# Optimization experiments

Measured on AMD Instinct MI355X. Metric: run time of the kernel, lower is better.

Reference implementation:

```python
import jax, jax.numpy as jnp
import numpy as np

N, D, BINS = 32768, 32, 16
SPLIT = D // 2                      # pyro spline_coupling default split
D2 = D - SPLIT
HID = 10 * D                        # pyro DenseNN default hidden dims
POUT = D2 * (3 * BINS + BINS - 1)   # widths, heights, derivatives, lambdas
BOUND = 3.0
MBW = 1e-3; MBH = 1e-3; MD = 1e-3; ML = 0.025
LOG2PI = float(np.log(2.0 * np.pi))


def _knots(lengths, lo, hi):
    # lengths [..., B] (positive, sums to 1) -> bin lengths and knot positions in [lo, hi]
    k = jnp.cumsum(lengths, axis=-1)
    k = jnp.concatenate([jnp.zeros_like(k[..., :1]), k], axis=-1)
    k = (hi - lo) * k + lo
    k = k.at[..., 0].set(lo)
    k = k.at[..., -1].set(hi)
    return k[..., 1:] - k[..., :-1], k


def rls_inverse(y, w_raw, h_raw, d_raw, l_raw):
    """Inverse monotonic rational-LINEAR spline (pyro order='linear').
    y: [N, Dp]; raw params broadcastable to [N, Dp, BINS] ([..., BINS-1] for d_raw).
    Returns x = spline^{-1}(y) and elementwise log|dx/dy|."""
    B = w_raw.shape[-1]
    w = MBW + (1.0 - MBW * B) * jax.nn.softmax(w_raw, axis=-1)
    h = MBH + (1.0 - MBH * B) * jax.nn.softmax(h_raw, axis=-1)
    d = MD + jax.nn.softplus(d_raw)
    lam = ML + (1.0 - 2.0 * ML) * jax.nn.sigmoid(l_raw)
    widths, cumw = _knots(w, -BOUND, BOUND)
    heights, cumh = _knots(h, -BOUND, BOUND)
    pad = jnp.full(d.shape[:-1] + (1,), 1.0 - MD, d.dtype)   # boundary derivatives
    d = jnp.concatenate([pad, d, pad], axis=-1)              # [..., B+1]

    bc = lambda t: jnp.broadcast_to(t, y.shape + (t.shape[-1],))
    widths, cumw, heights, cumh, d, lam = (bc(t) for t in (widths, cumw, heights, cumh, d, lam))

    inside = (y >= -BOUND) & (y <= BOUND)
    yc = jnp.clip(y, -BOUND, BOUND)
    # bin search on the y-knots (inverse pass)
    idx = jnp.clip(jnp.sum(yc[..., None] >= cumh, axis=-1) - 1, 0, B - 1)[..., None]
    take = lambda t: jnp.take_along_axis(t, idx, axis=-1)[..., 0]
    iw, icw, ih, ich = take(widths), take(cumw), take(heights), take(cumh)
    idel = ih / iw
    il = take(lam)
    idv, idvp1 = take(d[..., :-1]), take(d[..., 1:])

    wb = jnp.sqrt(idv / idvp1)                               # wa == 1
    wc = (il * idv + (1.0 - il) * wb * idvp1) / idel
    ya = ich
    yb = ih + ich
    ym = ((1.0 - il) * ya + il * wb * yb) / ((1.0 - il) + il * wb)

    left = yc <= ym
    num = jnp.where(left, il * (ya - yc),
                    (wc - il * wb) * yc + il * wb * yb - wc * ym)
    den = jnp.where(left, (wc - 1.0) * yc + ya - wc * ym,
                    (wc - wb) * yc + wb * yb - wc * ym)
    x = (num / den) * iw + icw
    dnum = jnp.where(left, wc * il * (ym - ya), wb * wc * (1.0 - il) * (yb - ym)) * iw
    ladj = jnp.log(dnum) - 2.0 * jnp.log(jnp.abs(den))
    return jnp.where(inside, x, y), jnp.where(inside, ladj, 0.0)


def coupling_inverse(y, lw, lh, ld, ll, W1, b1, W2, b2, W3, b3):
    y1, y2 = y[:, :SPLIT], y[:, SPLIT:]
    x1, l1 = rls_inverse(y1, lw, lh, ld, ll)                 # unconditional lower spline
    hdn = jax.nn.relu(x1 @ W1 + b1)
    hdn = jax.nn.relu(hdn @ W2 + b2)
    p = hdn @ W3 + b3                                        # hypernet -> upper spline params
    s0 = D2 * BINS; s1 = 2 * D2 * BINS; s2 = s1 + D2 * (BINS - 1)
    wr = p[:, :s0].reshape(-1, D2, BINS)
    hr = p[:, s0:s1].reshape(-1, D2, BINS)
    dr = p[:, s1:s2].reshape(-1, D2, BINS - 1)
    lr = p[:, s2:].reshape(-1, D2, BINS)
    x2, l2 = rls_inverse(y2, wr, hr, dr, lr)
    return jnp.concatenate([x1, x2], axis=-1), l1.sum(-1) + l2.sum(-1)


def _log_prob(data_samples, ds_means, ds_stds,
              t1_w, t1_h, t1_d, t1_l, t1_W1, t1_b1, t1_W2, t1_b2, t1_W3, t1_b3,
              t2_w, t2_h, t2_d, t2_l, t2_W1, t2_b1, t2_W2, t2_b2, t2_W3, t2_b3):
    scale = 10.0 * ds_stds
    z2 = (data_samples - ds_means) / scale                   # invert AffineTransform
    lp_aff = -jnp.sum(jnp.log(scale))                        # log|dz2/dy|
    z1, a2 = coupling_inverse(z2, t2_w, t2_h, t2_d, t2_l, t2_W1, t2_b1, t2_W2, t2_b2, t2_W3, t2_b3)
    z0, a1 = coupling_inverse(z1, t1_w, t1_h, t1_d, t1_l, t1_W1, t1_b1, t1_W2, t1_b2, t1_W3, t1_b3)
    base = -0.5 * jnp.sum(z0 * z0, axis=-1) - 0.5 * D * LOG2PI
    return base + a1 + a2 + lp_aff


def setup_inputs() -> dict:
    key = jax.random.key(0)
    ks = jax.random.split(key, 8)
    inp = {}
    inp["data_samples"] = jax.random.normal(ks[0], (N, D), jnp.float32)
    inp["ds_means"] = jax.random.normal(ks[1], (D,), jnp.float32)
    inp["ds_stds"] = jax.random.uniform(ks[2], (D,), jnp.float32, 0.5, 1.5)

    def spline_params(k):
        k1, k2, k3, k4 = jax.random.split(k, 4)
        return (0.5 * jax.random.normal(k1, (SPLIT, BINS), jnp.float32),
                0.5 * jax.random.normal(k2, (SPLIT, BINS), jnp.float32),
                0.5 * jax.random.normal(k3, (SPLIT, BINS - 1), jnp.float32),
                0.5 * jax.random.normal(k4, (SPLIT, BINS), jnp.float32))

    def nn_params(k):
        k1, k2, k3 = jax.random.split(k, 3)
        return (jax.random.normal(k1, (SPLIT, HID), jnp.float32) / np.sqrt(SPLIT),
                jnp.zeros((HID,), jnp.float32),
                jax.random.normal(k2, (HID, HID), jnp.float32) / np.sqrt(HID),
                jnp.zeros((HID,), jnp.float32),
                0.1 * jax.random.normal(k3, (HID, POUT), jnp.float32) / np.sqrt(HID),
                jnp.zeros((POUT,), jnp.float32))

    for t, ks_, kn_ in (("t1", ks[3], ks[5]), ("t2", ks[4], ks[6])):
        w, h, d, l = spline_params(ks_)
        inp[t + "_w"], inp[t + "_h"], inp[t + "_d"], inp[t + "_l"] = w, h, d, l
        W1, b1, W2, b2, W3, b3 = nn_params(kn_)
        inp[t + "_W1"], inp[t + "_b1"] = W1, b1
        inp[t + "_W2"], inp[t + "_b2"] = W2, b2
        inp[t + "_W3"], inp[t + "_b3"] = W3, b3
    return inp


def reference(data_samples, ds_means, ds_stds,
              t1_w, t1_h, t1_d, t1_l, t1_W1, t1_b1, t1_W2, t1_b2, t1_W3, t1_b3,
              t2_w, t2_h, t2_d, t2_l, t2_W1, t2_b1, t2_W2, t2_b2, t2_W3, t2_b3):
    return _log_prob(data_samples, ds_means, ds_stds,
                     t1_w, t1_h, t1_d, t1_l, t1_W1, t1_b1, t1_W2, t1_b2, t1_W3, t1_b3,
                     t2_w, t2_h, t2_d, t2_l, t2_W1, t2_b1, t2_W2, t2_b2, t2_W3, t2_b3)
```

## Files before the change

kernel.cpp:

```cpp
#include <hip/hip_runtime.h>
#include <math.h>

#define NROWS 32768
#define DD 32
#define HID 320
#define NBINS 16
#define BOUNDF 3.0f
#define MBWF 0.001f
#define MBHF 0.001f
#define MDF 0.001f
#define MLF 0.025f
#define LOG2PIF 1.8378770664093453f

#define WS_LP 0
#define WS_TBL 16
#define TBL_STRIDE 112
#define WS_B3P 4096
#define W2T_BYTE 32768
#define W3T_BYTE 442368

typedef __attribute__((ext_vector_type(8))) unsigned short ushort8_t;
typedef __attribute__((ext_vector_type(8))) __bf16 bf16x8;
typedef __attribute__((ext_vector_type(4))) float f32x4;

__device__ __forceinline__ unsigned short f2bf(float x) {
    unsigned u = __builtin_bit_cast(unsigned, x);
    return (unsigned short)((u + 0x7FFFu + ((u >> 16) & 1u)) >> 16);
}
__device__ __forceinline__ float bf2f(unsigned short s) {
    return __builtin_bit_cast(float, (unsigned)s << 16);
}
__device__ __forceinline__ f32x4 mfma_bf16(ushort8_t a, ushort8_t b, f32x4 c) {
    return __builtin_amdgcn_mfma_f32_16x16x32_bf16(
        __builtin_bit_cast(bf16x8, a), __builtin_bit_cast(bf16x8, b), c, 0, 0, 0);
}

__device__ __forceinline__ float softplus_precise(float x) {
    return (x > 0.f) ? (x + log1pf(expf(-x))) : log1pf(expf(x));
}
__device__ __forceinline__ float softplus_fast(float x) {
    return fmaxf(x, 0.f) + __logf(1.f + __expf(-fabsf(x)));
}

__device__ __forceinline__ void rls_core(float y, float iw, float icw, float ih, float ich,
                                         float il, float idv, float idvp1,
                                         float* xo, float* lo_) {
    bool inside = (y >= -BOUNDF) && (y <= BOUNDF);
    float yc = fminf(fmaxf(y, -BOUNDF), BOUNDF);
    float idel = ih / iw;
    float wb = sqrtf(idv / idvp1);
    float wc = (il * idv + (1.f - il) * wb * idvp1) / idel;
    float ya = ich;
    float yb = ih + ich;
    float ym = ((1.f - il) * ya + il * wb * yb) / ((1.f - il) + il * wb);
    bool left = (yc <= ym);
    float num = left ? (il * (ya - yc)) : ((wc - il * wb) * yc + il * wb * yb - wc * ym);
    float den = left ? ((wc - 1.f) * yc + ya - wc * ym) : ((wc - wb) * yc + wb * yb - wc * ym);
    float x = num / den * iw + icw;
    float dnum = (left ? (wc * il * (ym - ya)) : (wb * wc * (1.f - il) * (yb - ym))) * iw;
    float ladj = __logf(dnum) - 2.f * __logf(fabsf(den));
    *xo = inside ? x : y;
    *lo_ = inside ? ladj : 0.f;
}

__device__ __forceinline__ int colmap(int np) {
    int j = np >> 6, s = np & 63;
    if (s < 16) return j * 16 + s;
    if (s < 32) return 256 + j * 16 + (s - 16);
    if (s < 47) return 512 + j * 15 + (s - 32);
    if (s == 47) return -1;
    return 752 + j * 16 + (s - 48);
}

__global__ void prep_tables(const float* __restrict__ t1w, const float* __restrict__ t1h,
                            const float* __restrict__ t1d, const float* __restrict__ t1l,
                            const float* __restrict__ t2w, const float* __restrict__ t2h,
                            const float* __restrict__ t2d, const float* __restrict__ t2l,
                            const float* __restrict__ stds, float* __restrict__ ws) {
    int td = threadIdx.x;
    if (td == 32) {
        float lp = 0.f;
        for (int k = 0; k < DD; ++k) lp -= logf(10.f * stds[k]);
        ws[WS_LP] = lp;
    }
    if (td < 32) {
        int c = td >> 4, j = td & 15;
        const float* wr = (c == 0 ? t1w : t2w) + j * NBINS;
        const float* hr = (c == 0 ? t1h : t2h) + j * NBINS;
        const float* dr = (c == 0 ? t1d : t2d) + j * (NBINS - 1);
        const float* lr = (c == 0 ? t1l : t2l) + j * NBINS;
        float* tb = ws + WS_TBL + (c * 16 + j) * TBL_STRIDE;
        float mw = -1e30f, mh = -1e30f;
        for (int b = 0; b < NBINS; ++b) { mw = fmaxf(mw, wr[b]); mh = fmaxf(mh, hr[b]); }
        float sw = 0.f, sh = 0.f;
        for (int b = 0; b < NBINS; ++b) { sw += expf(wr[b] - mw); sh += expf(hr[b] - mh); }
        float fw = (1.f - NBINS * MBWF) / sw;
        float fh = (1.f - NBINS * MBHF) / sh;
        float kx[17], ky[17];
        kx[0] = -BOUNDF; ky[0] = -BOUNDF;
        float cw = 0.f, ch = 0.f;
        for (int b = 0; b < NBINS; ++b) {
            cw += MBWF + fw * expf(wr[b] - mw);
            ch += MBHF + fh * expf(hr[b] - mh);
            kx[b + 1] = 2.f * BOUNDF * cw - BOUNDF;
            ky[b + 1] = 2.f * BOUNDF * ch - BOUNDF;
        }
        kx[16] = BOUNDF; ky[16] = BOUNDF;
        for (int b = 0; b < 17; ++b) { tb[b] = ky[b]; tb[17 + b] = kx[b]; }
        tb[34] = 1.f - MDF;
        for (int b = 1; b <= 15; ++b) tb[34 + b] = MDF + softplus_precise(dr[b - 1]);
        tb[50] = 1.f - MDF;
        for (int b = 0; b < NBINS; ++b) {
            tb[51 + b] = kx[b + 1] - kx[b];
            tb[67 + b] = ky[b + 1] - ky[b];
            tb[83 + b] = MLF + (1.f - 2.f * MLF) / (1.f + expf(-lr[b]));
        }
    }
}

__global__ void prep_weights(const float* __restrict__ t2W2, const float* __restrict__ t1W2,
                             const float* __restrict__ t2W3, const float* __restrict__ t1W3,
                             const float* __restrict__ t2b3, const float* __restrict__ t1b3,
                             unsigned short* __restrict__ w2t, unsigned short* __restrict__ w3t,
                             float* __restrict__ b3p) {
    int id = blockIdx.x * 512 + threadIdx.x;
    if (id < 204800) {
        int c = id / 102400;
        int rem = id - c * 102400;
        int k = rem / 320, n = rem - k * 320;
        const float* W2 = c ? t1W2 : t2W2;
        w2t[c * 102400 + n * 320 + k] = f2bf(W2[k * 320 + n]);
    } else if (id < 860160) {
        int id2 = id - 204800;
        int c = id2 / 327680;
        int rem = id2 - c * 327680;
        int k = rem / 1024, np = rem - k * 1024;
        int col = colmap(np);
        const float* W3 = c ? t1W3 : t2W3;
        w3t[(size_t)c * 327680 + (size_t)np * 320 + k] =
            f2bf(col < 0 ? 0.f : W3[(size_t)k * 1008 + col]);
    } else if (id < 862208) {
        int idb = id - 860160;
        int c = idb / 1024, np = idb - c * 1024;
        int col = colmap(np);
        const float* b3 = c ? t1b3 : t2b3;
        b3p[c * 1024 + np] = (col < 0) ? 0.f : b3[col];
    }
}

__device__ __forceinline__ void coupling(
        int t, float (*zs)[33], float* lacc,
        unsigned short* h1b, unsigned short* h2b, unsigned short* pts,
        const float* __restrict__ tbl,
        const float* __restrict__ W1, const float* __restrict__ b1,
        const unsigned short* __restrict__ w2t, const float* __restrict__ b2,
        const unsigned short* __restrict__ w3t, const float* __restrict__ b3p) {
    const int l = t & 63, w = t >> 6;
    const int wm = w >> 2, wn = w & 3;

#pragma unroll
    for (int rep = 0; rep < 2; ++rep) {
        int row = (t >> 4) + rep * 32, jd = t & 15;
        float y1 = zs[row][jd];
        const float* tb = tbl + jd * TBL_STRIDE;
        float yc = fminf(fmaxf(y1, -BOUNDF), BOUNDF);
        int idx = 0;
#pragma unroll
        for (int b = 1; b <= 16; ++b) idx += (yc >= tb[b]) ? 1 : 0;
        if (idx > 15) idx = 15;
        float x, lv;
        rls_core(y1, tb[51 + idx], tb[17 + idx], tb[67 + idx], tb[idx],
                 tb[83 + idx], tb[34 + idx], tb[35 + idx], &x, &lv);
        zs[row][jd] = x;
        atomicAdd(&lacc[row], lv);
    }
    __syncthreads();

    {
        int cb = t & 63, rg = t >> 6;
        float acc[8][5];
#pragma unroll
        for (int j = 0; j < 5; ++j) {
            float bv = b1[cb + 64 * j];
#pragma unroll
            for (int i = 0; i < 8; ++i) acc[i][j] = bv;
        }
#pragma unroll
        for (int k = 0; k < 16; ++k) {
            float xv[8];
#pragma unroll
            for (int i = 0; i < 8; ++i) xv[i] = zs[rg * 8 + i][k];
#pragma unroll
            for (int j = 0; j < 5; ++j) {
                float wv = W1[k * HID + cb + 64 * j];
#pragma unroll
                for (int i = 0; i < 8; ++i) acc[i][j] += xv[i] * wv;
            }
        }
#pragma unroll
        for (int i = 0; i < 8; ++i) {
            int row = rg * 8 + i;
#pragma unroll
            for (int j = 0; j < 5; ++j) {
                int col = cb + 64 * j;
                h1b[row * 320 + (col ^ ((row & 7) << 3))] = f2bf(fmaxf(acc[i][j], 0.f));
            }
        }
    }
    __syncthreads();

    {
        const int mrow = wm * 32 + (l & 15);
        const int koff = (l >> 4) << 3;
        f32x4 acc[2][5];
        f32x4 z4 = {0.f, 0.f, 0.f, 0.f};
#pragma unroll
        for (int m = 0; m < 2; ++m)
#pragma unroll
            for (int nt = 0; nt < 5; ++nt) acc[m][nt] = z4;
#pragma unroll
        for (int kt = 0; kt < 10; ++kt) {
            int k = kt * 32 + koff;
            int kx = k ^ ((mrow & 7) << 3);
            ushort8_t a80 = *(const ushort8_t*)&h1b[mrow * 320 + kx];
            ushort8_t a81 = *(const ushort8_t*)&h1b[(mrow + 16) * 320 + kx];
#pragma unroll
            for (int nt = 0; nt < 5; ++nt) {
                int n = wn * 80 + nt * 16 + (l & 15);
                ushort8_t b8 = *(const ushort8_t*)&w2t[n * 320 + k];
                acc[0][nt] = mfma_bf16(a80, b8, acc[0][nt]);
                acc[1][nt] = mfma_bf16(a81, b8, acc[1][nt]);
            }
        }
#pragma unroll
        for (int m = 0; m < 2; ++m)
#pragma unroll
            for (int nt = 0; nt < 5; ++nt) {
                int n = wn * 80 + nt * 16 + (l & 15);
                float bias = b2[n];
#pragma unroll
                for (int r = 0; r < 4; ++r) {
                    int row = wm * 32 + m * 16 + ((l >> 4) << 2) + r;
                    float v = fmaxf(acc[m][nt][r] + bias, 0.f);
                    h2b[row * 320 + (n ^ ((row & 7) << 3))] = f2bf(v);
                }
            }
    }
    __syncthreads();

    for (int ch = 0; ch < 4; ++ch) {
        {
            const int mrow = wm * 32 + (l & 15);
            const int koff = (l >> 4) << 3;
            f32x4 acc[2][4];
            f32x4 z4 = {0.f, 0.f, 0.f, 0.f};
#pragma unroll
            for (int m = 0; m < 2; ++m)
#pragma unroll
                for (int nt = 0; nt < 4; ++nt) acc[m][nt] = z4;
#pragma unroll
            for (int kt = 0; kt < 10; ++kt) {
                int k = kt * 32 + koff;
                int kx = k ^ ((mrow & 7) << 3);
                ushort8_t a80 = *(const ushort8_t*)&h2b[mrow * 320 + kx];
                ushort8_t a81 = *(const ushort8_t*)&h2b[(mrow + 16) * 320 + kx];
#pragma unroll
                for (int nt = 0; nt < 4; ++nt) {
                    int ng = ch * 256 + wn * 64 + nt * 16 + (l & 15);
                    ushort8_t b8 = *(const ushort8_t*)&w3t[(size_t)ng * 320 + k];
                    acc[0][nt] = mfma_bf16(a80, b8, acc[0][nt]);
                    acc[1][nt] = mfma_bf16(a81, b8, acc[1][nt]);
                }
            }
#pragma unroll
            for (int m = 0; m < 2; ++m)
#pragma unroll
                for (int nt = 0; nt < 4; ++nt) {
                    int ng = ch * 256 + wn * 64 + nt * 16 + (l & 15);
                    float bias = b3p[ng];
                    int nl = wn * 64 + nt * 16 + (l & 15);
                    int js = nl >> 6;
#pragma unroll
                    for (int r = 0; r < 4; ++r) {
                        int row = wm * 32 + m * 16 + ((l >> 4) << 2) + r;
                        pts[row * 264 + (nl ^ (js << 3))] = f2bf(acc[m][nt][r] + bias);
                    }
                }
        }
        __syncthreads();
        if (t < 256) {
            int row = t >> 2, jl = t & 3;
            int j = ch * 4 + jl;
            float y = zs[row][16 + j];
            const unsigned short* pr = &pts[row * 264];
            const int base = jl * 64, xr = jl << 3;
            ushort8_t uw0 = *(const ushort8_t*)&pr[(base + 0) ^ xr];
            ushort8_t uw1 = *(const ushort8_t*)&pr[(base + 8) ^ xr];
            ushort8_t uh0 = *(const ushort8_t*)&pr[(base + 16) ^ xr];
            ushort8_t uh1 = *(const ushort8_t*)&pr[(base + 24) ^ xr];
            float mw = -1e30f, mh = -1e30f;
#pragma unroll
            for (int b = 0; b < 8; ++b) {
                mw = fmaxf(mw, fmaxf(bf2f(uw0[b]), bf2f(uw1[b])));
                mh = fmaxf(mh, fmaxf(bf2f(uh0[b]), bf2f(uh1[b])));
            }
            float sw = 0.f, sh = 0.f;
#pragma unroll
            for (int b = 0; b < 8; ++b) {
                sw += __expf(bf2f(uw0[b]) - mw) + __expf(bf2f(uw1[b]) - mw);
                sh += __expf(bf2f(uh0[b]) - mh) + __expf(bf2f(uh1[b]) - mh);
            }
            float fw = (1.f - NBINS * MBWF) / sw;
            float fh = (1.f - NBINS * MBHF) / sh;
            float yc = fminf(fmaxf(y, -BOUNDF), BOUNDF);
            float cw = -BOUNDF, chh = -BOUNDF, cumw = 0.f, cumh = 0.f;
            float iw = 1.f, icw = 0.f, ih = 1.f, ich = 0.f;
            int idx = 0;
#pragma unroll
            for (int b = 0; b < 16; ++b) {
                float wraw = (b < 8) ? bf2f(uw0[b]) : bf2f(uw1[b - 8]);
                float hraw = (b < 8) ? bf2f(uh0[b]) : bf2f(uh1[b - 8]);
                cumw += MBWF + fw * __expf(wraw - mw);
                cumh += MBHF + fh * __expf(hraw - mh);
                float cwn = (b == 15) ? BOUNDF : (2.f * BOUNDF * cumw - BOUNDF);
                float chn = (b == 15) ? BOUNDF : (2.f * BOUNDF * cumh - BOUNDF);
                bool sel = (yc >= chh);
                iw  = sel ? (cwn - cw)  : iw;
                icw = sel ? cw          : icw;
                ih  = sel ? (chn - chh) : ih;
                ich = sel ? chh         : ich;
                idx = sel ? b           : idx;
                cw = cwn; chh = chn;
            }
            float dm1 = bf2f(pr[(base + 32 + idx - 1) ^ xr]);
            float d0  = bf2f(pr[(base + 32 + idx) ^ xr]);
            float idv   = (idx == 0)  ? (1.f - MDF) : (MDF + softplus_fast(dm1));
            float idvp1 = (idx == 15) ? (1.f - MDF) : (MDF + softplus_fast(d0));
            float lraw = bf2f(pr[(base + 48 + idx) ^ xr]);
            float il = MLF + (1.f - 2.f * MLF) / (1.f + __expf(-lraw));
            float x, lv;
            rls_core(y, iw, icw, ih, ich, il, idv, idvp1, &x, &lv);
            zs[row][16 + j] = x;
            atomicAdd(&lacc[row], lv);
        }
        __syncthreads();
    }
}

__global__ __launch_bounds__(512, 2) void fused_kernel(
        const float* __restrict__ data, const float* __restrict__ means,
        const float* __restrict__ stds, const float* __restrict__ ws,
        const unsigned short* __restrict__ w2t, const unsigned short* __restrict__ w3t,
        const float* __restrict__ t2W1, const float* __restrict__ t2b1, const float* __restrict__ t2b2,
        const float* __restrict__ t1W1, const float* __restrict__ t1b1, const float* __restrict__ t1b2,
        float* __restrict__ out) {
    __shared__ float zs[64][33];
    __shared__ float lacc[64];
    __shared__ unsigned short h1b[64 * 320];
    __shared__ unsigned short h2b[64 * 320];
    __shared__ unsigned short pts[64 * 264];

    const int t = threadIdx.x;
    const int n0 = blockIdx.x * 64;

    {
        const float2* dp = (const float2*)(data + (size_t)n0 * DD);
#pragma unroll
        for (int rep = 0; rep < 2; ++rep) {
            int idx = t + rep * 512;
            float2 v = dp[idx];
            int row = idx >> 4, c = (idx & 15) * 2;
            zs[row][c]     = (v.x - means[c])     / (10.f * stds[c]);
            zs[row][c + 1] = (v.y - means[c + 1]) / (10.f * stds[c + 1]);
        }
        if (t < 64) lacc[t] = 0.f;
    }
    __syncthreads();

    const float* tbl_t1 = ws + WS_TBL;
    const float* tbl_t2 = ws + WS_TBL + 16 * TBL_STRIDE;
    const float* b3p    = ws + WS_B3P;

    coupling(t, zs, lacc, h1b, h2b, pts, tbl_t2, t2W1, t2b1,
             w2t, t2b2, w3t, b3p);
    coupling(t, zs, lacc, h1b, h2b, pts, tbl_t1, t1W1, t1b1,
             w2t + 102400, t1b2, w3t + 327680, b3p + 1024);

    if (t < 64) {
        float lp = ws[WS_LP];
        float ss = 0.f;
#pragma unroll
        for (int c = 0; c < DD; ++c) ss += zs[t][c] * zs[t][c];
        out[n0 + t] = -0.5f * ss - 16.f * LOG2PIF + lacc[t] + lp;
    }
}

extern "C" void kernel_launch(void* const* d_in, const int* in_sizes, int n_in,
                              void* d_out, int out_size, void* d_ws, size_t ws_size,
                              hipStream_t stream) {
    const float* data  = (const float*)d_in[0];
    const float* means = (const float*)d_in[1];
    const float* stds  = (const float*)d_in[2];
    const float* t1w = (const float*)d_in[3];
    const float* t1h = (const float*)d_in[4];
    const float* t1d = (const float*)d_in[5];
    const float* t1l = (const float*)d_in[6];
    const float* t1W1 = (const float*)d_in[7];
    const float* t1b1 = (const float*)d_in[8];
    const float* t1W2 = (const float*)d_in[9];
    const float* t1b2 = (const float*)d_in[10];
    const float* t1W3 = (const float*)d_in[11];
    const float* t1b3 = (const float*)d_in[12];
    const float* t2w = (const float*)d_in[13];
    const float* t2h = (const float*)d_in[14];
    const float* t2d = (const float*)d_in[15];
    const float* t2l = (const float*)d_in[16];
    const float* t2W1 = (const float*)d_in[17];
    const float* t2b1 = (const float*)d_in[18];
    const float* t2W2 = (const float*)d_in[19];
    const float* t2b2 = (const float*)d_in[20];
    const float* t2W3 = (const float*)d_in[21];
    const float* t2b3 = (const float*)d_in[22];

    float* ws = (float*)d_ws;
    unsigned short* w2t = (unsigned short*)((char*)d_ws + W2T_BYTE);
    unsigned short* w3t = (unsigned short*)((char*)d_ws + W3T_BYTE);
    float* b3p = ws + WS_B3P;

    prep_tables<<<1, 64, 0, stream>>>(t1w, t1h, t1d, t1l, t2w, t2h, t2d, t2l, stds, ws);
    prep_weights<<<1684, 512, 0, stream>>>(t2W2, t1W2, t2W3, t1W3, t2b3, t1b3, w2t, w3t, b3p);
    fused_kernel<<<NROWS / 64, 512, 0, stream>>>(
        data, means, stds, ws, w2t, w3t,
        t2W1, t2b1, t2b2, t1W1, t1b1, t1b2, (float*)d_out);
}
```

Before: 422.1 us.

## Double-buffer spline parameter tiles to overlap layer-3 GEMM with spline evaluation

Splits the layer-3 GEMM and the rational-linear spline evaluation into separate helper functions and double-buffers the parameter tile in shared memory (pts0/pts1). GEMM chunk c+1 is now issued before the spline pass for chunk c with no barrier between them, so the MFMA work of some waves can overlap the scalar spline work of others. This cuts the barriers per coupling from 8 to 5. The cost is about 33KB more LDS per block, which may threaten the 2-blocks-per-CU occupancy.

Measured after the change: 383.5 us. -9.1%, faster.

```diff
diff --git a/kernel.cpp b/kernel.cpp
--- a/kernel.cpp
+++ b/kernel.cpp
@@ -148,9 +148,112 @@
     }
 }
 
+__device__ __forceinline__ void gemm_chunk(
+        int ch, int t, const unsigned short* h2b, unsigned short* pb,
+        const unsigned short* __restrict__ w3t, const float* __restrict__ b3p) {
+    const int l = t & 63, w = t >> 6;
+    const int wm = w >> 2, wn = w & 3;
+    const int mrow = wm * 32 + (l & 15);
+    const int koff = (l >> 4) << 3;
+    f32x4 acc[2][4];
+    f32x4 z4 = {0.f, 0.f, 0.f, 0.f};
+#pragma unroll
+    for (int m = 0; m < 2; ++m)
+#pragma unroll
+        for (int nt = 0; nt < 4; ++nt) acc[m][nt] = z4;
+#pragma unroll
+    for (int kt = 0; kt < 10; ++kt) {
+        int k = kt * 32 + koff;
+        int kx = k ^ ((mrow & 7) << 3);
+        ushort8_t a80 = *(const ushort8_t*)&h2b[mrow * 320 + kx];
+        ushort8_t a81 = *(const ushort8_t*)&h2b[(mrow + 16) * 320 + kx];
+#pragma unroll
+        for (int nt = 0; nt < 4; ++nt) {
+            int ng = ch * 256 + wn * 64 + nt * 16 + (l & 15);
+            ushort8_t b8 = *(const ushort8_t*)&w3t[(size_t)ng * 320 + k];
+            acc[0][nt] = mfma_bf16(a80, b8, acc[0][nt]);
+            acc[1][nt] = mfma_bf16(a81, b8, acc[1][nt]);
+        }
+    }
+#pragma unroll
+    for (int m = 0; m < 2; ++m)
+#pragma unroll
+        for (int nt = 0; nt < 4; ++nt) {
+            int ng = ch * 256 + wn * 64 + nt * 16 + (l & 15);
+            float bias = b3p[ng];
+            int nl = wn * 64 + nt * 16 + (l & 15);
+            int js = nl >> 6;
+#pragma unroll
+            for (int r = 0; r < 4; ++r) {
+                int row = wm * 32 + m * 16 + ((l >> 4) << 2) + r;
+                pb[row * 264 + (nl ^ (js << 3))] = f2bf(acc[m][nt][r] + bias);
+            }
+        }
+}
+
+__device__ __forceinline__ void spline2_chunk(
+        int ch, int t, float (*zs)[33], float* lacc, const unsigned short* pb) {
+    if (t < 256) {
+        int row = t >> 2, jl = t & 3;
+        int j = ch * 4 + jl;
+        float y = zs[row][16 + j];
+        const unsigned short* pr = &pb[row * 264];
+        const int base = jl * 64, xr = jl << 3;
+        ushort8_t uw0 = *(const ushort8_t*)&pr[(base + 0) ^ xr];
+        ushort8_t uw1 = *(const ushort8_t*)&pr[(base + 8) ^ xr];
+        ushort8_t uh0 = *(const ushort8_t*)&pr[(base + 16) ^ xr];
+        ushort8_t uh1 = *(const ushort8_t*)&pr[(base + 24) ^ xr];
+        float mw = -1e30f, mh = -1e30f;
+#pragma unroll
+        for (int b = 0; b < 8; ++b) {
+            mw = fmaxf(mw, fmaxf(bf2f(uw0[b]), bf2f(uw1[b])));
+            mh = fmaxf(mh, fmaxf(bf2f(uh0[b]), bf2f(uh1[b])));
+        }
+        float sw = 0.f, sh = 0.f;
+#pragma unroll
+        for (int b = 0; b < 8; ++b) {
+            sw += __expf(bf2f(uw0[b]) - mw) + __expf(bf2f(uw1[b]) - mw);
+            sh += __expf(bf2f(uh0[b]) - mh) + __expf(bf2f(uh1[b]) - mh);
+        }
+        float fw = (1.f - NBINS * MBWF) / sw;
+        float fh = (1.f - NBINS * MBHF) / sh;
+        float yc = fminf(fmaxf(y, -BOUNDF), BOUNDF);
+        float cw = -BOUNDF, chh = -BOUNDF, cumw = 0.f, cumh = 0.f;
+        float iw = 1.f, icw = 0.f, ih = 1.f, ich = 0.f;
+        int idx = 0;
+#pragma unroll
+        for (int b = 0; b < 16; ++b) {
+            float wraw = (b < 8) ? bf2f(uw0[b]) : bf2f(uw1[b - 8]);
+            float hraw = (b < 8) ? bf2f(uh0[b]) : bf2f(uh1[b - 8]);
+            cumw += MBWF + fw * __expf(wraw - mw);
+            cumh += MBHF + fh * __expf(hraw - mh);
+            float cwn = (b == 15) ? BOUNDF : (2.f * BOUNDF * cumw - BOUNDF);
+            float chn = (b == 15) ? BOUNDF : (2.f * BOUNDF * cumh - BOUNDF);
+            bool sel = (yc >= chh);
+            iw  = sel ? (cwn - cw)  : iw;
+            icw = sel ? cw          : icw;
+            ih  = sel ? (chn - chh) : ih;
+            ich = sel ? chh         : ich;
+            idx = sel ? b           : idx;
+            cw = cwn; chh = chn;
+        }
+        float dm1 = bf2f(pr[(base + 32 + idx - 1) ^ xr]);
+        float d0  = bf2f(pr[(base + 32 + idx) ^ xr]);
+        float idv   = (idx == 0)  ? (1.f - MDF) : (MDF + softplus_fast(dm1));
+        float idvp1 = (idx == 15) ? (1.f - MDF) : (MDF + softplus_fast(d0));
+        float lraw = bf2f(pr[(base + 48 + idx) ^ xr]);
+        float il = MLF + (1.f - 2.f * MLF) / (1.f + __expf(-lraw));
+        float x, lv;
+        rls_core(y, iw, icw, ih, ich, il, idv, idvp1, &x, &lv);
+        zs[row][16 + j] = x;
+        atomicAdd(&lacc[row], lv);
+    }
+}
+
 __device__ __forceinline__ void coupling(
         int t, float (*zs)[33], float* lacc,
-        unsigned short* h1b, unsigned short* h2b, unsigned short* pts,
+        unsigned short* h1b, unsigned short* h2b,
+        unsigned short* pts0, unsigned short* pts1,
         const float* __restrict__ tbl,
         const float* __restrict__ W1, const float* __restrict__ b1,
         const unsigned short* __restrict__ w2t, const float* __restrict__ b2,
@@ -248,103 +351,19 @@
     }
     __syncthreads();
 
-    for (int ch = 0; ch < 4; ++ch) {
-        {
-            const int mrow = wm * 32 + (l & 15);
-            const int koff = (l >> 4) << 3;
-            f32x4 acc[2][4];
-            f32x4 z4 = {0.f, 0.f, 0.f, 0.f};
-#pragma unroll
-            for (int m = 0; m < 2; ++m)
-#pragma unroll
-                for (int nt = 0; nt < 4; ++nt) acc[m][nt] = z4;
-#pragma unroll
-            for (int kt = 0; kt < 10; ++kt) {
-                int k = kt * 32 + koff;
-                int kx = k ^ ((mrow & 7) << 3);
-                ushort8_t a80 = *(const ushort8_t*)&h2b[mrow * 320 + kx];
-                ushort8_t a81 = *(const ushort8_t*)&h2b[(mrow + 16) * 320 + kx];
-#pragma unroll
-                for (int nt = 0; nt < 4; ++nt) {
-                    int ng = ch * 256 + wn * 64 + nt * 16 + (l & 15);
-                    ushort8_t b8 = *(const ushort8_t*)&w3t[(size_t)ng * 320 + k];
-                    acc[0][nt] = mfma_bf16(a80, b8, acc[0][nt]);
-                    acc[1][nt] = mfma_bf16(a81, b8, acc[1][nt]);
-                }
-            }
-#pragma unroll
-            for (int m = 0; m < 2; ++m)
-#pragma unroll
-                for (int nt = 0; nt < 4; ++nt) {
-                    int ng = ch * 256 + wn * 64 + nt * 16 + (l & 15);
-                    float bias = b3p[ng];
-                    int nl = wn * 64 + nt * 16 + (l & 15);
-                    int js = nl >> 6;
-#pragma unroll
-                    for (int r = 0; r < 4; ++r) {
-                        int row = wm * 32 + m * 16 + ((l >> 4) << 2) + r;
-                        pts[row * 264 + (nl ^ (js << 3))] = f2bf(acc[m][nt][r] + bias);
-                    }
-                }
-        }
-        __syncthreads();
-        if (t < 256) {
-            int row = t >> 2, jl = t & 3;
-            int j = ch * 4 + jl;
-            float y = zs[row][16 + j];
-            const unsigned short* pr = &pts[row * 264];
-            const int base = jl * 64, xr = jl << 3;
-            ushort8_t uw0 = *(const ushort8_t*)&pr[(base + 0) ^ xr];
-            ushort8_t uw1 = *(const ushort8_t*)&pr[(base + 8) ^ xr];
-            ushort8_t uh0 = *(const ushort8_t*)&pr[(base + 16) ^ xr];
-            ushort8_t uh1 = *(const ushort8_t*)&pr[(base + 24) ^ xr];
-            float mw = -1e30f, mh = -1e30f;
-#pragma unroll
-            for (int b = 0; b < 8; ++b) {
-                mw = fmaxf(mw, fmaxf(bf2f(uw0[b]), bf2f(uw1[b])));
-                mh = fmaxf(mh, fmaxf(bf2f(uh0[b]), bf2f(uh1[b])));
-            }
-            float sw = 0.f, sh = 0.f;
-#pragma unroll
-            for (int b = 0; b < 8; ++b) {
-                sw += __expf(bf2f(uw0[b]) - mw) + __expf(bf2f(uw1[b]) - mw);
-                sh += __expf(bf2f(uh0[b]) - mh) + __expf(bf2f(uh1[b]) - mh);
-            }
-            float fw = (1.f - NBINS * MBWF) / sw;
-            float fh = (1.f - NBINS * MBHF) / sh;
-            float yc = fminf(fmaxf(y, -BOUNDF), BOUNDF);
-            float cw = -BOUNDF, chh = -BOUNDF, cumw = 0.f, cumh = 0.f;
-            float iw = 1.f, icw = 0.f, ih = 1.f, ich = 0.f;
-            int idx = 0;
-#pragma unroll
-            for (int b = 0; b < 16; ++b) {
-                float wraw = (b < 8) ? bf2f(uw0[b]) : bf2f(uw1[b - 8]);
-                float hraw = (b < 8) ? bf2f(uh0[b]) : bf2f(uh1[b - 8]);
-                cumw += MBWF + fw * __expf(wraw - mw);
-                cumh += MBHF + fh * __expf(hraw - mh);
-                float cwn = (b == 15) ? BOUNDF : (2.f * BOUNDF * cumw - BOUNDF);
-                float chn = (b == 15) ? BOUNDF : (2.f * BOUNDF * cumh - BOUNDF);
-                bool sel = (yc >= chh);
-                iw  = sel ? (cwn - cw)  : iw;
-                icw = sel ? cw          : icw;
-                ih  = sel ? (chn - chh) : ih;
-                ich = sel ? chh         : ich;
-                idx = sel ? b           : idx;
-                cw = cwn; chh = chn;
-            }
-            float dm1 = bf2f(pr[(base + 32 + idx - 1) ^ xr]);
-            float d0  = bf2f(pr[(base + 32 + idx) ^ xr]);
-            float idv   = (idx == 0)  ? (1.f - MDF) : (MDF + softplus_fast(dm1));
-            float idvp1 = (idx == 15) ? (1.f - MDF) : (MDF + softplus_fast(d0));
-            float lraw = bf2f(pr[(base + 48 + idx) ^ xr]);
-            float il = MLF + (1.f - 2.f * MLF) / (1.f + __expf(-lraw));
-            float x, lv;
-            rls_core(y, iw, icw, ih, ich, il, idv, idvp1, &x, &lv);
-            zs[row][16 + j] = x;
-            atomicAdd(&lacc[row], lv);
-        }
-        __syncthreads();
-    }
+    gemm_chunk(0, t, h2b, pts0, w3t, b3p);
+    __syncthreads();
+    gemm_chunk(1, t, h2b, pts1, w3t, b3p);
+    spline2_chunk(0, t, zs, lacc, pts0);
+    __syncthreads();
+    gemm_chunk(2, t, h2b, pts0, w3t, b3p);
+    spline2_chunk(1, t, zs, lacc, pts1);
+    __syncthreads();
+    gemm_chunk(3, t, h2b, pts1, w3t, b3p);
+    spline2_chunk(2, t, zs, lacc, pts0);
+    __syncthreads();
+    spline2_chunk(3, t, zs, lacc, pts1);
+    __syncthreads();
 }
 
 __global__ __launch_bounds__(512, 2) void fused_kernel(
@@ -358,7 +377,8 @@
     __shared__ float lacc[64];
     __shared__ unsigned short h1b[64 * 320];
     __shared__ unsigned short h2b[64 * 320];
-    __shared__ unsigned short pts[64 * 264];
+    __shared__ unsigned short pts0[64 * 264];
+    __shared__ unsigned short pts1[64 * 264];
 
     const int t = threadIdx.x;
     const int n0 = blockIdx.x * 64;
@@ -381,9 +401,9 @@
     const float* tbl_t2 = ws + WS_TBL + 16 * TBL_STRIDE;
     const float* b3p    = ws + WS_B3P;
 
-    coupling(t, zs, lacc, h1b, h2b, pts, tbl_t2, t2W1, t2b1,
+    coupling(t, zs, lacc, h1b, h2b, pts0, pts1, tbl_t2, t2W1, t2b1,
              w2t, t2b2, w3t, b3p);
-    coupling(t, zs, lacc, h1b, h2b, pts, tbl_t1, t1W1, t1b1,
+    coupling(t, zs, lacc, h1b, h2b, pts0, pts1, tbl_t1, t1W1, t1b1,
              w2t + 102400, t1b2, w3t + 327680, b3p + 1024);
 
     if (t < 64) {
```
